# Performance work log

Hardware: AMD Instinct MI355X
Metric: run time of the kernel (lower is better)

## Reference

```python
import jax, jax.numpy as jnp
import numpy as np

B, C, F_IN, F_OUT = 4096, 63, 250, 250
NEG_SLOPE = 0.2  # GATConv default negative_slope


def setup_inputs() -> dict:
    key = jax.random.key(0)
    ks = jax.random.split(key, 5)
    return {
        "x": jax.random.normal(ks[0], (B, 1, C, F_IN), dtype=jnp.float32),
        "W": jax.random.normal(ks[1], (F_IN, F_OUT), dtype=jnp.float32) / np.sqrt(F_IN),
        "att_src": jax.random.normal(ks[2], (F_OUT,), dtype=jnp.float32) / np.sqrt(F_OUT),
        "att_dst": jax.random.normal(ks[3], (F_OUT,), dtype=jnp.float32) / np.sqrt(F_OUT),
        "bias": jax.random.normal(ks[4], (F_OUT,), dtype=jnp.float32) * 0.01,
    }


def reference(x, W, att_src, att_dst, bias):
    # x: [B, 1, C, F_in] -> per-batch graph of C=63 nodes, fully connected
    # (all i!=j edges plus GATConv's default self-loops => dense C x C attention).
    h = jnp.einsum("bcf,fo->bco", x[:, 0], W)          # [B, C, F_out] node embeddings
    a_s = jnp.einsum("bco,o->bc", h, att_src)           # per-source score
    a_d = jnp.einsum("bco,o->bc", h, att_dst)           # per-destination score
    # e[b, dst, src] = leakyrelu(a_s[src] + a_d[dst]); softmax over sources per dst
    e = jax.nn.leaky_relu(a_s[:, None, :] + a_d[:, :, None], NEG_SLOPE)  # [B, C, C]
    alpha = jax.nn.softmax(e, axis=-1)
    out = jnp.einsum("bds,bso->bdo", alpha, h) + bias   # [B, C, F_out]
    return out[:, None]                                  # [B, 1, C, F_out]
```

## Files before the change

### kernel.cpp

```cpp
#include <hip/hip_runtime.h>
#include <hip/hip_bf16.h>

typedef __bf16 bf16;
typedef __attribute__((ext_vector_type(8))) __bf16 bf16x8;
typedef __attribute__((ext_vector_type(4))) __bf16 bf16x4;
typedef __attribute__((ext_vector_type(2))) __bf16 bf16x2;
typedef __attribute__((ext_vector_type(4))) float f32x4;

#define C_NODES 63
#define F_DIM   250
#define NEG_SLOPE 0.2f

#define OFF_AS    32000
#define OFF_AD    32256
#define OFF_ALPHA 32768
#define LDS_BYTES 40960

__device__ __forceinline__ int swz(int a) { return a ^ ((a >> 3) & 0x70); }
__device__ __forceinline__ int swzA(int a) {
    return a ^ ((((a >> 8) & 3) ^ ((a >> 10) & 3)) << 4) ^ (((a >> 12) & 1) << 6);
}

extern "C" __global__ __launch_bounds__(256)
void gat_prep(const float* __restrict__ W, const float* __restrict__ att_src,
              const float* __restrict__ att_dst, bf16* __restrict__ Wp) {
    int i = blockIdx.x * 256 + threadIdx.x;
    int tile = i >> 9;
    int ln   = (i >> 3) & 63;
    int j    = i & 7;
    int kt = tile >> 4, nt = tile & 15;
    int k = kt * 32 + (ln >> 4) * 8 + j;
    int n = nt * 16 + (ln & 15);
    float v = 0.f;
    if (k < F_DIM) {
        if (n < F_DIM) {
            v = W[k * F_DIM + n];
        } else if (n == F_DIM || n == F_DIM + 1) {
            const float* att = (n == F_DIM) ? att_src : att_dst;
            float s = 0.f;
            for (int o = 0; o < F_DIM; ++o) s = fmaf(W[k * F_DIM + o], att[o], s);
            v = s;
        }
    }
    Wp[i] = (bf16)v;
}

extern "C" __global__ __launch_bounds__(512, 8)
void gat_main(const float* __restrict__ x, const bf16* __restrict__ Wp,
              const float* __restrict__ bias, float* __restrict__ out)
{
    __shared__ __align__(16) unsigned char smem[LDS_BYTES];
    const int tid  = threadIdx.x;
    const int lane = tid & 63;
    const int w    = tid >> 6;
    const int b    = blockIdx.x;
    const int fl   = lane & 15;
    const int fh   = lane >> 4;

    const bf16x8* wpv = (const bf16x8*)Wp;

    if (tid < 64) {
        int base = swzA((((tid >> 4) * 8 + 7) << 10) + (48 + (tid & 15)) * 16);
        *(unsigned int*)(smem + base + 4) = 0u;
        *(unsigned long long*)(smem + base + 8) = 0ull;
    } else if (tid < 96) {
        int idx = tid - 64;
        int base = swzA(((24 + (idx >> 2)) << 10) + ((((idx & 3) << 4) | 15) * 16));
        *(f32x4*)(smem + base) = (f32x4){0.f, 0.f, 0.f, 0.f};
    }

    {
        const float* xb = x + (size_t)b * (C_NODES * F_DIM);
#pragma unroll
        for (int it = 0; it < 4; ++it) {
            int idx = tid + it * 512;
            if (idx < 2016) {
                int r = idx >> 5, g = idx & 31;
                const float* src = xb + r * F_DIM + g * 8;
                int dl = (r & 15) | ((g & 3) << 4);
                int base = swzA((((r >> 4) * 8 + (g >> 2)) << 10) + dl * 16);
                if (g < 31) {
                    float2 v0 = *(const float2*)(src);
                    float2 v1 = *(const float2*)(src + 2);
                    float2 v2 = *(const float2*)(src + 4);
                    float2 v3 = *(const float2*)(src + 6);
                    bf16x8 pk = { (bf16)v0.x, (bf16)v0.y, (bf16)v1.x, (bf16)v1.y,
                                  (bf16)v2.x, (bf16)v2.y, (bf16)v3.x, (bf16)v3.y };
                    *(bf16x8*)(smem + base) = pk;
                } else {
                    float2 v0 = *(const float2*)(src);
                    bf16x2 pk = { (bf16)v0.x, (bf16)v0.y };
                    *(bf16x2*)(smem + base) = pk;
                }
            }
        }
    }
    __syncthreads();

    f32x4 acc[4][2];
#pragma unroll
    for (int mt = 0; mt < 4; ++mt) {
        acc[mt][0] = (f32x4){0.f, 0.f, 0.f, 0.f};
        acc[mt][1] = (f32x4){0.f, 0.f, 0.f, 0.f};
    }
#pragma unroll 1
    for (int kt = 0; kt < 8; ++kt) {
        bf16x8 bw0 = wpv[(kt * 16 + w * 2)     * 64 + lane];
        bf16x8 bw1 = wpv[(kt * 16 + w * 2 + 1) * 64 + lane];
#pragma unroll
        for (int mt = 0; mt < 4; ++mt) {
            bf16x8 af = *(const bf16x8*)(smem + swzA(((mt * 8 + kt) << 10) + lane * 16));
            acc[mt][0] = __builtin_amdgcn_mfma_f32_16x16x32_bf16(af, bw0, acc[mt][0], 0, 0, 0);
            acc[mt][1] = __builtin_amdgcn_mfma_f32_16x16x32_bf16(af, bw1, acc[mt][1], 0, 0, 0);
        }
    }
    __syncthreads();

    {
#pragma unroll
        for (int mt = 0; mt < 4; ++mt) {
            int s0 = mt * 16 + fh * 4;
#pragma unroll
            for (int nti = 0; nti < 2; ++nti) {
                int f = w * 32 + nti * 16 + fl;
                if (f < F_DIM) {
                    f32x4 v = acc[mt][nti];
                    bf16x4 hv = { (bf16)v.x, (bf16)v.y, (bf16)v.z, (bf16)v.w };
                    *(bf16x4*)(smem + swz(f * 128 + s0 * 2)) = hv;
                }
            }
        }
        if (w == 7 && (fl == 10 || fl == 11)) {
            float* dst = (float*)(smem + (fl == 10 ? OFF_AS : OFF_AD));
#pragma unroll
            for (int mt = 0; mt < 4; ++mt) {
                f32x4 v = acc[mt][1];
#pragma unroll
                for (int i = 0; i < 4; ++i) dst[mt * 16 + fh * 4 + i] = v[i];
            }
        }
    }
    __syncthreads();

    {
        const float* AS  = (const float*)(smem + OFF_AS);
        const float* ADp = (const float*)(smem + OFF_AD);
        int d = tid >> 3;
        int c = tid & 7;
        float ad_v = ADp[d];
        f32x4 a0 = *(const f32x4*)(AS + c * 8);
        f32x4 a1 = *(const f32x4*)(AS + c * 8 + 4);
        float p[8];
#pragma unroll
        for (int k = 0; k < 4; ++k) {
            float e;
            e = a0[k] + ad_v; p[k]     = (e > 0.f) ? e : NEG_SLOPE * e;
            e = a1[k] + ad_v; p[4 + k] = (e > 0.f) ? e : NEG_SLOPE * e;
        }
        if (c == 7) p[7] = -3.0e38f;
        float md = p[0];
#pragma unroll
        for (int k = 1; k < 8; ++k) md = fmaxf(md, p[k]);
        md = fmaxf(md, __shfl_xor(md, 1));
        md = fmaxf(md, __shfl_xor(md, 2));
        md = fmaxf(md, __shfl_xor(md, 4));
        float sum = 0.f;
#pragma unroll
        for (int k = 0; k < 8; ++k) { p[k] = __expf(p[k] - md); sum += p[k]; }
        sum += __shfl_xor(sum, 1);
        sum += __shfl_xor(sum, 2);
        sum += __shfl_xor(sum, 4);
        float rz = 1.f / sum;
        bf16x8 pk;
#pragma unroll
        for (int k = 0; k < 8; ++k) pk[k] = (bf16)(p[k] * rz);
        *(bf16x8*)(smem + swz(OFF_ALPHA + d * 128 + c * 16)) = pk;
    }
    __syncthreads();

    f32x4 acc2[4][2];
#pragma unroll
    for (int mt = 0; mt < 4; ++mt) {
        acc2[mt][0] = (f32x4){0.f, 0.f, 0.f, 0.f};
        acc2[mt][1] = (f32x4){0.f, 0.f, 0.f, 0.f};
    }
#pragma unroll 1
    for (int ks = 0; ks < 2; ++ks) {
        int kk = ks * 32 + fh * 8;
        bf16x8 hbf0, hbf1;
        {
            int f0 = w * 32 + fl;
            int f1 = f0 + 16;
            hbf0 = *(const bf16x8*)(smem + swz(f0 * 128 + kk * 2));
            hbf1 = *(const bf16x8*)(smem + swz(f1 * 128 + kk * 2));
        }
#pragma unroll
        for (int mt = 0; mt < 4; ++mt) {
            bf16x8 aal = *(const bf16x8*)(smem + swz(OFF_ALPHA + (mt * 16 + fl) * 128 + kk * 2));
            acc2[mt][0] = __builtin_amdgcn_mfma_f32_16x16x32_bf16(aal, hbf0, acc2[mt][0], 0, 0, 0);
            acc2[mt][1] = __builtin_amdgcn_mfma_f32_16x16x32_bf16(aal, hbf1, acc2[mt][1], 0, 0, 0);
        }
    }

    float bv[2];
#pragma unroll
    for (int nti = 0; nti < 2; ++nti) {
        int f = w * 32 + nti * 16 + fl;
        bv[nti] = (f < F_DIM) ? bias[f] : 0.f;
    }
    float* ob = out + (size_t)b * (C_NODES * F_DIM);
#pragma unroll
    for (int mt = 0; mt < 4; ++mt) {
#pragma unroll
        for (int i = 0; i < 4; ++i) {
            int r = mt * 16 + fh * 4 + i;
            if (r < C_NODES) {
#pragma unroll
                for (int nti = 0; nti < 2; ++nti) {
                    int f = w * 32 + nti * 16 + fl;
                    if (f < F_DIM) ob[r * F_DIM + f] = acc2[mt][nti][i] + bv[nti];
                }
            }
        }
    }
}

extern "C" void kernel_launch(void* const* d_in, const int* in_sizes, int n_in,
                              void* d_out, int out_size, void* d_ws, size_t ws_size,
                              hipStream_t stream) {
    const float* x       = (const float*)d_in[0];
    const float* W       = (const float*)d_in[1];
    const float* att_src = (const float*)d_in[2];
    const float* att_dst = (const float*)d_in[3];
    const float* bias    = (const float*)d_in[4];
    float* out = (float*)d_out;
    bf16* Wp = (bf16*)d_ws;

    gat_prep<<<256, 256, 0, stream>>>(W, att_src, att_dst, Wp);
    gat_main<<<4096, 512, 0, stream>>>(x, Wp, bias, out);
}
```

Measured before the change: 145.5 us.

## Keep h and attention in registers via cross-lane shuffles, dropping LDS round trips

```diff
diff --git a/kernel.cpp b/kernel.cpp
--- a/kernel.cpp
+++ b/kernel.cpp
@@ -3,20 +3,16 @@
 
 typedef __bf16 bf16;
 typedef __attribute__((ext_vector_type(8))) __bf16 bf16x8;
-typedef __attribute__((ext_vector_type(4))) __bf16 bf16x4;
 typedef __attribute__((ext_vector_type(2))) __bf16 bf16x2;
 typedef __attribute__((ext_vector_type(4))) float f32x4;
+typedef __attribute__((ext_vector_type(4))) unsigned int uint4v;
 
 #define C_NODES 63
 #define F_DIM   250
 #define NEG_SLOPE 0.2f
 
-#define OFF_AS    32000
-#define OFF_AD    32256
-#define OFF_ALPHA 32768
-#define LDS_BYTES 40960
-
-__device__ __forceinline__ int swz(int a) { return a ^ ((a >> 3) & 0x70); }
+#define LDS_BYTES 32768
+
 __device__ __forceinline__ int swzA(int a) {
     return a ^ ((((a >> 8) & 3) ^ ((a >> 10) & 3)) << 4) ^ (((a >> 12) & 1) << 6);
 }
@@ -45,7 +41,7 @@
     Wp[i] = (bf16)v;
 }
 
-extern "C" __global__ __launch_bounds__(512, 8)
+extern "C" __global__ __launch_bounds__(512, 4)
 void gat_main(const float* __restrict__ x, const bf16* __restrict__ Wp,
               const float* __restrict__ bias, float* __restrict__ out)
 {
@@ -84,13 +80,13 @@
                     float2 v1 = *(const float2*)(src + 2);
                     float2 v2 = *(const float2*)(src + 4);
                     float2 v3 = *(const float2*)(src + 6);
-                    bf16x8 pk = { (bf16)v0.x, (bf16)v0.y, (bf16)v1.x, (bf16)v1.y,
-                                  (bf16)v2.x, (bf16)v2.y, (bf16)v3.x, (bf16)v3.y };
-                    *(bf16x8*)(smem + base) = pk;
+                    bf16x8 pk8 = { (bf16)v0.x, (bf16)v0.y, (bf16)v1.x, (bf16)v1.y,
+                                   (bf16)v2.x, (bf16)v2.y, (bf16)v3.x, (bf16)v3.y };
+                    *(bf16x8*)(smem + base) = pk8;
                 } else {
                     float2 v0 = *(const float2*)(src);
-                    bf16x2 pk = { (bf16)v0.x, (bf16)v0.y };
-                    *(bf16x2*)(smem + base) = pk;
+                    bf16x2 pk2 = { (bf16)v0.x, (bf16)v0.y };
+                    *(bf16x2*)(smem + base) = pk2;
                 }
             }
         }
@@ -98,107 +94,120 @@
     __syncthreads();
 
     f32x4 acc[4][2];
+    f32x4 acc15[4];
 #pragma unroll
     for (int mt = 0; mt < 4; ++mt) {
         acc[mt][0] = (f32x4){0.f, 0.f, 0.f, 0.f};
         acc[mt][1] = (f32x4){0.f, 0.f, 0.f, 0.f};
+        acc15[mt]  = (f32x4){0.f, 0.f, 0.f, 0.f};
     }
 #pragma unroll 1
     for (int kt = 0; kt < 8; ++kt) {
         bf16x8 bw0 = wpv[(kt * 16 + w * 2)     * 64 + lane];
         bf16x8 bw1 = wpv[(kt * 16 + w * 2 + 1) * 64 + lane];
+        bf16x8 bwS = wpv[(kt * 16 + 15)        * 64 + lane];
 #pragma unroll
         for (int mt = 0; mt < 4; ++mt) {
             bf16x8 af = *(const bf16x8*)(smem + swzA(((mt * 8 + kt) << 10) + lane * 16));
             acc[mt][0] = __builtin_amdgcn_mfma_f32_16x16x32_bf16(af, bw0, acc[mt][0], 0, 0, 0);
             acc[mt][1] = __builtin_amdgcn_mfma_f32_16x16x32_bf16(af, bw1, acc[mt][1], 0, 0, 0);
-        }
-    }
-    __syncthreads();
-
+            acc15[mt]  = __builtin_amdgcn_mfma_f32_16x16x32_bf16(af, bwS, acc15[mt], 0, 0, 0);
+        }
+    }
+
+    unsigned int pk[4][2][2];
+#pragma unroll
+    for (int mt = 0; mt < 4; ++mt)
+#pragma unroll
+        for (int nti = 0; nti < 2; ++nti) {
+            f32x4 v = acc[mt][nti];
+            bf16x2 p0 = { (bf16)v.x, (bf16)v.y };
+            bf16x2 p1 = { (bf16)v.z, (bf16)v.w };
+            pk[mt][nti][0] = __builtin_bit_cast(unsigned int, p0);
+            pk[mt][nti][1] = __builtin_bit_cast(unsigned int, p1);
+        }
+
+    const int LA = ((fh & 1) << 5) + fl;
+    const int LB = LA + 16;
+    const bool fhHi = (fh & 2) != 0;
+    uint4v hb[2][2];
+#pragma unroll
+    for (int nti = 0; nti < 2; ++nti)
+#pragma unroll
+        for (int kt2 = 0; kt2 < 2; ++kt2) {
+            unsigned int u[4];
+#pragma unroll
+            for (int h = 0; h < 2; ++h) {
+                unsigned int a0 = __shfl(pk[kt2 * 2][nti][h],     LA);
+                unsigned int a1 = __shfl(pk[kt2 * 2 + 1][nti][h], LA);
+                u[h] = fhHi ? a1 : a0;
+                unsigned int b0 = __shfl(pk[kt2 * 2][nti][h],     LB);
+                unsigned int b1 = __shfl(pk[kt2 * 2 + 1][nti][h], LB);
+                u[2 + h] = fhHi ? b1 : b0;
+            }
+            hb[nti][kt2] = (uint4v){u[0], u[1], u[2], u[3]};
+        }
+
+    float asv[16];
+#pragma unroll
+    for (int kt2 = 0; kt2 < 2; ++kt2)
+#pragma unroll
+        for (int j = 0; j < 8; ++j) {
+            int Ls = (((fh & 1) * 2 + (j >> 2)) << 4) + 10;
+            float c0 = __shfl(acc15[kt2 * 2][j & 3],     Ls);
+            float c1 = __shfl(acc15[kt2 * 2 + 1][j & 3], Ls);
+            asv[kt2 * 8 + j] = fhHi ? c1 : c0;
+        }
+    float adv[4];
     {
+        int Ld = ((fl >> 2) << 4) + 11;
 #pragma unroll
         for (int mt = 0; mt < 4; ++mt) {
-            int s0 = mt * 16 + fh * 4;
-#pragma unroll
-            for (int nti = 0; nti < 2; ++nti) {
-                int f = w * 32 + nti * 16 + fl;
-                if (f < F_DIM) {
-                    f32x4 v = acc[mt][nti];
-                    bf16x4 hv = { (bf16)v.x, (bf16)v.y, (bf16)v.z, (bf16)v.w };
-                    *(bf16x4*)(smem + swz(f * 128 + s0 * 2)) = hv;
-                }
-            }
-        }
-        if (w == 7 && (fl == 10 || fl == 11)) {
-            float* dst = (float*)(smem + (fl == 10 ? OFF_AS : OFF_AD));
-#pragma unroll
-            for (int mt = 0; mt < 4; ++mt) {
-                f32x4 v = acc[mt][1];
-#pragma unroll
-                for (int i = 0; i < 4; ++i) dst[mt * 16 + fh * 4 + i] = v[i];
-            }
-        }
-    }
-    __syncthreads();
-
-    {
-        const float* AS  = (const float*)(smem + OFF_AS);
-        const float* ADp = (const float*)(smem + OFF_AD);
-        int d = tid >> 3;
-        int c = tid & 7;
-        float ad_v = ADp[d];
-        f32x4 a0 = *(const f32x4*)(AS + c * 8);
-        f32x4 a1 = *(const f32x4*)(AS + c * 8 + 4);
-        float p[8];
-#pragma unroll
-        for (int k = 0; k < 4; ++k) {
-            float e;
-            e = a0[k] + ad_v; p[k]     = (e > 0.f) ? e : NEG_SLOPE * e;
-            e = a1[k] + ad_v; p[4 + k] = (e > 0.f) ? e : NEG_SLOPE * e;
-        }
-        if (c == 7) p[7] = -3.0e38f;
+            float t0 = __shfl(acc15[mt][0], Ld);
+            float t1 = __shfl(acc15[mt][1], Ld);
+            float t2 = __shfl(acc15[mt][2], Ld);
+            float t3 = __shfl(acc15[mt][3], Ld);
+            float s01 = (fl & 1) ? t1 : t0;
+            float s23 = (fl & 1) ? t3 : t2;
+            adv[mt] = (fl & 2) ? s23 : s01;
+        }
+    }
+
+    f32x4 acc2[4][2];
+#pragma unroll
+    for (int mt = 0; mt < 4; ++mt) {
+        float p[16];
+#pragma unroll
+        for (int k = 0; k < 16; ++k) {
+            float e = asv[k] + adv[mt];
+            p[k] = (e > 0.f) ? e : NEG_SLOPE * e;
+        }
+        if (fh == 3) p[15] = -3.0e38f;
         float md = p[0];
 #pragma unroll
-        for (int k = 1; k < 8; ++k) md = fmaxf(md, p[k]);
-        md = fmaxf(md, __shfl_xor(md, 1));
-        md = fmaxf(md, __shfl_xor(md, 2));
-        md = fmaxf(md, __shfl_xor(md, 4));
+        for (int k = 1; k < 16; ++k) md = fmaxf(md, p[k]);
+        md = fmaxf(md, __shfl_xor(md, 16));
+        md = fmaxf(md, __shfl_xor(md, 32));
         float sum = 0.f;
 #pragma unroll
-        for (int k = 0; k < 8; ++k) { p[k] = __expf(p[k] - md); sum += p[k]; }
-        sum += __shfl_xor(sum, 1);
-        sum += __shfl_xor(sum, 2);
-        sum += __shfl_xor(sum, 4);
+        for (int k = 0; k < 16; ++k) { p[k] = __expf(p[k] - md); sum += p[k]; }
+        sum += __shfl_xor(sum, 16);
+        sum += __shfl_xor(sum, 32);
         float rz = 1.f / sum;
-        bf16x8 pk;
-#pragma unroll
-        for (int k = 0; k < 8; ++k) pk[k] = (bf16)(p[k] * rz);
-        *(bf16x8*)(smem + swz(OFF_ALPHA + d * 128 + c * 16)) = pk;
-    }
-    __syncthreads();
-
-    f32x4 acc2[4][2];
-#pragma unroll
-    for (int mt = 0; mt < 4; ++mt) {
+        bf16x8 aal0, aal1;
+#pragma unroll
+        for (int k = 0; k < 8; ++k) {
+            aal0[k] = (bf16)(p[k] * rz);
+            aal1[k] = (bf16)(p[8 + k] * rz);
+        }
         acc2[mt][0] = (f32x4){0.f, 0.f, 0.f, 0.f};
         acc2[mt][1] = (f32x4){0.f, 0.f, 0.f, 0.f};
-    }
-#pragma unroll 1
-    for (int ks = 0; ks < 2; ++ks) {
-        int kk = ks * 32 + fh * 8;
-        bf16x8 hbf0, hbf1;
-        {
-            int f0 = w * 32 + fl;
-            int f1 = f0 + 16;
-            hbf0 = *(const bf16x8*)(smem + swz(f0 * 128 + kk * 2));
-            hbf1 = *(const bf16x8*)(smem + swz(f1 * 128 + kk * 2));
-        }
-#pragma unroll
-        for (int mt = 0; mt < 4; ++mt) {
-            bf16x8 aal = *(const bf16x8*)(smem + swz(OFF_ALPHA + (mt * 16 + fl) * 128 + kk * 2));
-            acc2[mt][0] = __builtin_amdgcn_mfma_f32_16x16x32_bf16(aal, hbf0, acc2[mt][0], 0, 0, 0);
-            acc2[mt][1] = __builtin_amdgcn_mfma_f32_16x16x32_bf16(aal, hbf1, acc2[mt][1], 0, 0, 0);
+#pragma unroll
+        for (int nti = 0; nti < 2; ++nti) {
+            bf16x8 h0 = __builtin_bit_cast(bf16x8, hb[nti][0]);
+            bf16x8 h1 = __builtin_bit_cast(bf16x8, hb[nti][1]);
+            acc2[mt][nti] = __builtin_amdgcn_mfma_f32_16x16x32_bf16(aal0, h0, acc2[mt][nti], 0, 0, 0);
+            acc2[mt][nti] = __builtin_amdgcn_mfma_f32_16x16x32_bf16(aal1, h1, acc2[mt][nti], 0, 0, 0);
         }
     }
 
```

Result: slower. 164.5 us (+13.1%).

## Process eight batches per persistent block with register prefetch of next x

Applied to the files above, without the earlier changes.

```diff
diff --git a/kernel.cpp b/kernel.cpp
--- a/kernel.cpp
+++ b/kernel.cpp
@@ -10,15 +10,24 @@
 #define C_NODES 63
 #define F_DIM   250
 #define NEG_SLOPE 0.2f
-
-#define OFF_AS    32000
-#define OFF_AD    32256
-#define OFF_ALPHA 32768
-#define LDS_BYTES 40960
+#define BS 8
+
+#define AFR_B     0
+#define HSB       32768
+#define OFF_AS    64768
+#define OFF_AD    65024
+#define ALPHA_B   65280
+#define LDS_BYTES 73472
 
 __device__ __forceinline__ int swz(int a) { return a ^ ((a >> 3) & 0x70); }
 __device__ __forceinline__ int swzA(int a) {
     return a ^ ((((a >> 8) & 3) ^ ((a >> 10) & 3)) << 4) ^ (((a >> 12) & 1) << 6);
+}
+
+__device__ __forceinline__ void barrier_lds() {
+    asm volatile("s_waitcnt lgkmcnt(0)" ::: "memory");
+    __builtin_amdgcn_s_barrier();
+    __builtin_amdgcn_sched_barrier(0);
 }
 
 extern "C" __global__ __launch_bounds__(256)
@@ -45,7 +54,7 @@
     Wp[i] = (bf16)v;
 }
 
-extern "C" __global__ __launch_bounds__(512, 8)
+extern "C" __global__ __launch_bounds__(512, 4)
 void gat_main(const float* __restrict__ x, const bf16* __restrict__ Wp,
               const float* __restrict__ bias, float* __restrict__ out)
 {
@@ -53,9 +62,9 @@
     const int tid  = threadIdx.x;
     const int lane = tid & 63;
     const int w    = tid >> 6;
-    const int b    = blockIdx.x;
     const int fl   = lane & 15;
     const int fh   = lane >> 4;
+    const int b0   = blockIdx.x * BS;
 
     const bf16x8* wpv = (const bf16x8*)Wp;
 
@@ -69,8 +78,12 @@
         *(f32x4*)(smem + base) = (f32x4){0.f, 0.f, 0.f, 0.f};
     }
 
+    float bv0, bv1;
+    { int f = w * 32 + fl;      bv0 = (f < F_DIM) ? bias[f] : 0.f;
+      f += 16;                  bv1 = (f < F_DIM) ? bias[f] : 0.f; }
+
     {
-        const float* xb = x + (size_t)b * (C_NODES * F_DIM);
+        const float* xb = x + (size_t)b0 * (C_NODES * F_DIM);
 #pragma unroll
         for (int it = 0; it < 4; ++it) {
             int idx = tid + it * 512;
@@ -84,39 +97,61 @@
                     float2 v1 = *(const float2*)(src + 2);
                     float2 v2 = *(const float2*)(src + 4);
                     float2 v3 = *(const float2*)(src + 6);
-                    bf16x8 pk = { (bf16)v0.x, (bf16)v0.y, (bf16)v1.x, (bf16)v1.y,
-                                  (bf16)v2.x, (bf16)v2.y, (bf16)v3.x, (bf16)v3.y };
-                    *(bf16x8*)(smem + base) = pk;
+                    bf16x8 pk8 = { (bf16)v0.x, (bf16)v0.y, (bf16)v1.x, (bf16)v1.y,
+                                   (bf16)v2.x, (bf16)v2.y, (bf16)v3.x, (bf16)v3.y };
+                    *(bf16x8*)(smem + base) = pk8;
                 } else {
                     float2 v0 = *(const float2*)(src);
-                    bf16x2 pk = { (bf16)v0.x, (bf16)v0.y };
-                    *(bf16x2*)(smem + base) = pk;
-                }
-            }
-        }
-    }
-    __syncthreads();
-
-    f32x4 acc[4][2];
-#pragma unroll
-    for (int mt = 0; mt < 4; ++mt) {
-        acc[mt][0] = (f32x4){0.f, 0.f, 0.f, 0.f};
-        acc[mt][1] = (f32x4){0.f, 0.f, 0.f, 0.f};
-    }
+                    bf16x2 pk2 = { (bf16)v0.x, (bf16)v0.y };
+                    *(bf16x2*)(smem + base) = pk2;
+                }
+            }
+        }
+    }
+
+    float2 pf[4][4];
+    {
+        const float* xb = x + (size_t)(b0 + 1) * (C_NODES * F_DIM);
+#pragma unroll
+        for (int it = 0; it < 4; ++it) {
+            int idx = tid + it * 512;
+            if (idx < 2016) {
+                int r = idx >> 5, g = idx & 31;
+                const float* src = xb + r * F_DIM + g * 8;
+                pf[it][0] = *(const float2*)(src);
+                if (g < 31) {
+                    pf[it][1] = *(const float2*)(src + 2);
+                    pf[it][2] = *(const float2*)(src + 4);
+                    pf[it][3] = *(const float2*)(src + 6);
+                }
+            }
+        }
+    }
+    barrier_lds();
+
 #pragma unroll 1
-    for (int kt = 0; kt < 8; ++kt) {
-        bf16x8 bw0 = wpv[(kt * 16 + w * 2)     * 64 + lane];
-        bf16x8 bw1 = wpv[(kt * 16 + w * 2 + 1) * 64 + lane];
+    for (int i = 0; i < BS; ++i) {
+        const int b = b0 + i;
+
+        f32x4 acc[4][2];
 #pragma unroll
         for (int mt = 0; mt < 4; ++mt) {
-            bf16x8 af = *(const bf16x8*)(smem + swzA(((mt * 8 + kt) << 10) + lane * 16));
-            acc[mt][0] = __builtin_amdgcn_mfma_f32_16x16x32_bf16(af, bw0, acc[mt][0], 0, 0, 0);
-            acc[mt][1] = __builtin_amdgcn_mfma_f32_16x16x32_bf16(af, bw1, acc[mt][1], 0, 0, 0);
-        }
-    }
-    __syncthreads();
-
-    {
+            acc[mt][0] = (f32x4){0.f, 0.f, 0.f, 0.f};
+            acc[mt][1] = (f32x4){0.f, 0.f, 0.f, 0.f};
+        }
+#pragma unroll 1
+        for (int kt = 0; kt < 8; ++kt) {
+            bf16x8 bw0 = wpv[(kt * 16 + w * 2)     * 64 + lane];
+            bf16x8 bw1 = wpv[(kt * 16 + w * 2 + 1) * 64 + lane];
+#pragma unroll
+            for (int mt = 0; mt < 4; ++mt) {
+                bf16x8 af = *(const bf16x8*)(smem + swzA(((mt * 8 + kt) << 10) + lane * 16));
+                acc[mt][0] = __builtin_amdgcn_mfma_f32_16x16x32_bf16(af, bw0, acc[mt][0], 0, 0, 0);
+                acc[mt][1] = __builtin_amdgcn_mfma_f32_16x16x32_bf16(af, bw1, acc[mt][1], 0, 0, 0);
+            }
+        }
+        barrier_lds();
+
 #pragma unroll
         for (int mt = 0; mt < 4; ++mt) {
             int s0 = mt * 16 + fh * 4;
@@ -126,7 +161,7 @@
                 if (f < F_DIM) {
                     f32x4 v = acc[mt][nti];
                     bf16x4 hv = { (bf16)v.x, (bf16)v.y, (bf16)v.z, (bf16)v.w };
-                    *(bf16x4*)(smem + swz(f * 128 + s0 * 2)) = hv;
+                    *(bf16x4*)(smem + swz(HSB + f * 128 + s0 * 2)) = hv;
                 }
             }
         }
@@ -136,89 +171,114 @@
             for (int mt = 0; mt < 4; ++mt) {
                 f32x4 v = acc[mt][1];
 #pragma unroll
-                for (int i = 0; i < 4; ++i) dst[mt * 16 + fh * 4 + i] = v[i];
-            }
-        }
-    }
-    __syncthreads();
-
-    {
-        const float* AS  = (const float*)(smem + OFF_AS);
-        const float* ADp = (const float*)(smem + OFF_AD);
-        int d = tid >> 3;
-        int c = tid & 7;
-        float ad_v = ADp[d];
-        f32x4 a0 = *(const f32x4*)(AS + c * 8);
-        f32x4 a1 = *(const f32x4*)(AS + c * 8 + 4);
-        float p[8];
-#pragma unroll
-        for (int k = 0; k < 4; ++k) {
-            float e;
-            e = a0[k] + ad_v; p[k]     = (e > 0.f) ? e : NEG_SLOPE * e;
-            e = a1[k] + ad_v; p[4 + k] = (e > 0.f) ? e : NEG_SLOPE * e;
-        }
-        if (c == 7) p[7] = -3.0e38f;
-        float md = p[0];
-#pragma unroll
-        for (int k = 1; k < 8; ++k) md = fmaxf(md, p[k]);
-        md = fmaxf(md, __shfl_xor(md, 1));
-        md = fmaxf(md, __shfl_xor(md, 2));
-        md = fmaxf(md, __shfl_xor(md, 4));
-        float sum = 0.f;
-#pragma unroll
-        for (int k = 0; k < 8; ++k) { p[k] = __expf(p[k] - md); sum += p[k]; }
-        sum += __shfl_xor(sum, 1);
-        sum += __shfl_xor(sum, 2);
-        sum += __shfl_xor(sum, 4);
-        float rz = 1.f / sum;
-        bf16x8 pk;
-#pragma unroll
-        for (int k = 0; k < 8; ++k) pk[k] = (bf16)(p[k] * rz);
-        *(bf16x8*)(smem + swz(OFF_ALPHA + d * 128 + c * 16)) = pk;
-    }
-    __syncthreads();
-
-    f32x4 acc2[4][2];
-#pragma unroll
-    for (int mt = 0; mt < 4; ++mt) {
-        acc2[mt][0] = (f32x4){0.f, 0.f, 0.f, 0.f};
-        acc2[mt][1] = (f32x4){0.f, 0.f, 0.f, 0.f};
-    }
+                for (int q = 0; q < 4; ++q) dst[mt * 16 + fh * 4 + q] = v[q];
+            }
+        }
+        if (i + 1 < BS) {
+#pragma unroll
+            for (int it = 0; it < 4; ++it) {
+                int idx = tid + it * 512;
+                if (idx < 2016) {
+                    int r = idx >> 5, g = idx & 31;
+                    int dl = (r & 15) | ((g & 3) << 4);
+                    int base = swzA((((r >> 4) * 8 + (g >> 2)) << 10) + dl * 16);
+                    if (g < 31) {
+                        bf16x8 pk8 = { (bf16)pf[it][0].x, (bf16)pf[it][0].y,
+                                       (bf16)pf[it][1].x, (bf16)pf[it][1].y,
+                                       (bf16)pf[it][2].x, (bf16)pf[it][2].y,
+                                       (bf16)pf[it][3].x, (bf16)pf[it][3].y };
+                        *(bf16x8*)(smem + base) = pk8;
+                    } else {
+                        bf16x2 pk2 = { (bf16)pf[it][0].x, (bf16)pf[it][0].y };
+                        *(bf16x2*)(smem + base) = pk2;
+                    }
+                }
+            }
+            if (i + 2 < BS) {
+                const float* xb = x + (size_t)(b0 + i + 2) * (C_NODES * F_DIM);
+#pragma unroll
+                for (int it = 0; it < 4; ++it) {
+                    int idx = tid + it * 512;
+                    if (idx < 2016) {
+                        int r = idx >> 5, g = idx & 31;
+                        const float* src = xb + r * F_DIM + g * 8;
+                        pf[it][0] = *(const float2*)(src);
+                        if (g < 31) {
+                            pf[it][1] = *(const float2*)(src + 2);
+                            pf[it][2] = *(const float2*)(src + 4);
+                            pf[it][3] = *(const float2*)(src + 6);
+                        }
+                    }
+                }
+            }
+        }
+        barrier_lds();
+
+        {
+            const float* AS  = (const float*)(smem + OFF_AS);
+            const float* ADp = (const float*)(smem + OFF_AD);
+            int d = tid >> 3;
+            int c = tid & 7;
+            float ad_v = ADp[d];
+            f32x4 a0 = *(const f32x4*)(AS + c * 8);
+            f32x4 a1 = *(const f32x4*)(AS + c * 8 + 4);
+            float p[8];
+#pragma unroll
+            for (int k = 0; k < 4; ++k) {
+                float e;
+                e = a0[k] + ad_v; p[k]     = (e > 0.f) ? e : NEG_SLOPE * e;
+                e = a1[k] + ad_v; p[4 + k] = (e > 0.f) ? e : NEG_SLOPE * e;
+            }
+            if (c == 7) p[7] = -3.0e38f;
+            float md = p[0];
+#pragma unroll
+            for (int k = 1; k < 8; ++k) md = fmaxf(md, p[k]);
+            md = fmaxf(md, __shfl_xor(md, 1));
+            md = fmaxf(md, __shfl_xor(md, 2));
+            md = fmaxf(md, __shfl_xor(md, 4));
+            float sum = 0.f;
+#pragma unroll
+            for (int k = 0; k < 8; ++k) { p[k] = __expf(p[k] - md); sum += p[k]; }
+            sum += __shfl_xor(sum, 1);
+            sum += __shfl_xor(sum, 2);
+            sum += __shfl_xor(sum, 4);
+            float rz = 1.f / sum;
+            bf16x8 pk;
+#pragma unroll
+            for (int k = 0; k < 8; ++k) pk[k] = (bf16)(p[k] * rz);
+            *(bf16x8*)(smem + swz(ALPHA_B + d * 128 + c * 16)) = pk;
+        }
+        barrier_lds();
+
+        f32x4 acc2[4][2];
+#pragma unroll
+        for (int mt = 0; mt < 4; ++mt) {
+            acc2[mt][0] = (f32x4){0.f, 0.f, 0.f, 0.f};
+            acc2[mt][1] = (f32x4){0.f, 0.f, 0.f, 0.f};
+        }
 #pragma unroll 1
-    for (int ks = 0; ks < 2; ++ks) {
-        int kk = ks * 32 + fh * 8;
-        bf16x8 hbf0, hbf1;
-        {
-            int f0 = w * 32 + fl;
-            int f1 = f0 + 16;
-            hbf0 = *(const bf16x8*)(smem + swz(f0 * 128 + kk * 2));
-            hbf1 = *(const bf16x8*)(smem + swz(f1 * 128 + kk * 2));
-        }
+        for (int ks = 0; ks < 2; ++ks) {
+            int kk = ks * 32 + fh * 8;
+            bf16x8 hbf0 = *(const bf16x8*)(smem + swz(HSB + (w * 32 + fl)      * 128 + kk * 2));
+            bf16x8 hbf1 = *(const bf16x8*)(smem + swz(HSB + (w * 32 + fl + 16) * 128 + kk * 2));
+#pragma unroll
+            for (int mt = 0; mt < 4; ++mt) {
+                bf16x8 aal = *(const bf16x8*)(smem + swz(ALPHA_B + (mt * 16 + fl) * 128 + kk * 2));
+                acc2[mt][0] = __builtin_amdgcn_mfma_f32_16x16x32_bf16(aal, hbf0, acc2[mt][0], 0, 0, 0);
+                acc2[mt][1] = __builtin_amdgcn_mfma_f32_16x16x32_bf16(aal, hbf1, acc2[mt][1], 0, 0, 0);
+            }
+        }
+        float* ob = out + (size_t)b * (C_NODES * F_DIM);
 #pragma unroll
         for (int mt = 0; mt < 4; ++mt) {
-            bf16x8 aal = *(const bf16x8*)(smem + swz(OFF_ALPHA + (mt * 16 + fl) * 128 + kk * 2));
-            acc2[mt][0] = __builtin_amdgcn_mfma_f32_16x16x32_bf16(aal, hbf0, acc2[mt][0], 0, 0, 0);
-            acc2[mt][1] = __builtin_amdgcn_mfma_f32_16x16x32_bf16(aal, hbf1, acc2[mt][1], 0, 0, 0);
-        }
-    }
-
-    float bv[2];
-#pragma unroll
-    for (int nti = 0; nti < 2; ++nti) {
-        int f = w * 32 + nti * 16 + fl;
-        bv[nti] = (f < F_DIM) ? bias[f] : 0.f;
-    }
-    float* ob = out + (size_t)b * (C_NODES * F_DIM);
-#pragma unroll
-    for (int mt = 0; mt < 4; ++mt) {
-#pragma unroll
-        for (int i = 0; i < 4; ++i) {
-            int r = mt * 16 + fh * 4 + i;
-            if (r < C_NODES) {
-#pragma unroll
-                for (int nti = 0; nti < 2; ++nti) {
-                    int f = w * 32 + nti * 16 + fl;
-                    if (f < F_DIM) ob[r * F_DIM + f] = acc2[mt][nti][i] + bv[nti];
+#pragma unroll
+            for (int q = 0; q < 4; ++q) {
+                int r = mt * 16 + fh * 4 + q;
+                if (r < C_NODES) {
+                    int f = w * 32 + fl;
+                    ob[r * F_DIM + f] = acc2[mt][0][q] + bv0;
+                    f += 16;
+                    if (f < F_DIM) ob[r * F_DIM + f] = acc2[mt][1][q] + bv1;
                 }
             }
         }
@@ -237,5 +297,5 @@
     bf16* Wp = (bf16*)d_ws;
 
     gat_prep<<<256, 256, 0, stream>>>(W, att_src, att_dst, Wp);
-    gat_main<<<4096, 512, 0, stream>>>(x, Wp, bias, out);
-}
+    gat_main<<<512, 512, 0, stream>>>(x, Wp, bias, out);
+}
```

After: 207.6 us. +42.6%, slower.

## Process 8 batches per block with async global-to-LDS prefetch of next x

Applied to the files above, without the earlier changes.

```diff
diff --git a/kernel.cpp b/kernel.cpp
--- a/kernel.cpp
+++ b/kernel.cpp
@@ -3,22 +3,34 @@
 
 typedef __bf16 bf16;
 typedef __attribute__((ext_vector_type(8))) __bf16 bf16x8;
-typedef __attribute__((ext_vector_type(4))) __bf16 bf16x4;
 typedef __attribute__((ext_vector_type(2))) __bf16 bf16x2;
 typedef __attribute__((ext_vector_type(4))) float f32x4;
+typedef __attribute__((ext_vector_type(4))) unsigned int uint4v;
 
 #define C_NODES 63
 #define F_DIM   250
 #define NEG_SLOPE 0.2f
-
-#define OFF_AS    32000
-#define OFF_AD    32256
-#define OFF_ALPHA 32768
-#define LDS_BYTES 40960
+#define BS 8
+
+#define ROWB      1040
+#define SLAB      0
+#define OFF_AS    65536
+#define OFF_AD    65792
+#define ALPHA_B   66048
+#define LDS_BYTES 74240
 
 __device__ __forceinline__ int swz(int a) { return a ^ ((a >> 3) & 0x70); }
-__device__ __forceinline__ int swzA(int a) {
-    return a ^ ((((a >> 8) & 3) ^ ((a >> 10) & 3)) << 4) ^ (((a >> 12) & 1) << 6);
+
+typedef const __attribute__((address_space(1))) void* gas_t;
+typedef __attribute__((address_space(3))) void* las_t;
+__device__ __forceinline__ void dma16(const void* g, void* l) {
+    __builtin_amdgcn_global_load_lds((gas_t)g, (las_t)l, 16, 0, 0);
+}
+
+__device__ __forceinline__ void bar_lgkm() {
+    asm volatile("s_waitcnt lgkmcnt(0)" ::: "memory");
+    __builtin_amdgcn_s_barrier();
+    __builtin_amdgcn_sched_barrier(0);
 }
 
 extern "C" __global__ __launch_bounds__(256)
@@ -45,7 +57,7 @@
     Wp[i] = (bf16)v;
 }
 
-extern "C" __global__ __launch_bounds__(512, 8)
+extern "C" __global__ __launch_bounds__(512, 4)
 void gat_main(const float* __restrict__ x, const bf16* __restrict__ Wp,
               const float* __restrict__ bias, float* __restrict__ out)
 {
@@ -53,81 +65,79 @@
     const int tid  = threadIdx.x;
     const int lane = tid & 63;
     const int w    = tid >> 6;
-    const int b    = blockIdx.x;
     const int fl   = lane & 15;
     const int fh   = lane >> 4;
+    const int b0   = blockIdx.x * BS;
 
     const bf16x8* wpv = (const bf16x8*)Wp;
 
-    if (tid < 64) {
-        int base = swzA((((tid >> 4) * 8 + 7) << 10) + (48 + (tid & 15)) * 16);
-        *(unsigned int*)(smem + base + 4) = 0u;
-        *(unsigned long long*)(smem + base + 8) = 0ull;
-    } else if (tid < 96) {
-        int idx = tid - 64;
-        int base = swzA(((24 + (idx >> 2)) << 10) + ((((idx & 3) << 4) | 15) * 16));
-        *(f32x4*)(smem + base) = (f32x4){0.f, 0.f, 0.f, 0.f};
+    float bv0, bv1;
+    { int f = w * 32 + fl;      bv0 = (f < F_DIM) ? bias[f] : 0.f;
+      f += 16;                  bv1 = (f < F_DIM) ? bias[f] : 0.f; }
+
+    if (tid < 63) {
+        *(unsigned long long*)(smem + SLAB + tid * ROWB + 1000) = 0ull;
+        *(f32x4*)(smem + SLAB + tid * ROWB + 1008) = (f32x4){0.f, 0.f, 0.f, 0.f};
     }
 
     {
-        const float* xb = x + (size_t)b * (C_NODES * F_DIM);
-#pragma unroll
-        for (int it = 0; it < 4; ++it) {
-            int idx = tid + it * 512;
-            if (idx < 2016) {
-                int r = idx >> 5, g = idx & 31;
-                const float* src = xb + r * F_DIM + g * 8;
-                int dl = (r & 15) | ((g & 3) << 4);
-                int base = swzA((((r >> 4) * 8 + (g >> 2)) << 10) + dl * 16);
-                if (g < 31) {
-                    float2 v0 = *(const float2*)(src);
-                    float2 v1 = *(const float2*)(src + 2);
-                    float2 v2 = *(const float2*)(src + 4);
-                    float2 v3 = *(const float2*)(src + 6);
-                    bf16x8 pk = { (bf16)v0.x, (bf16)v0.y, (bf16)v1.x, (bf16)v1.y,
-                                  (bf16)v2.x, (bf16)v2.y, (bf16)v3.x, (bf16)v3.y };
-                    *(bf16x8*)(smem + base) = pk;
+        const float* xb = x + (size_t)b0 * (C_NODES * F_DIM);
+        float2 tl = {0.f, 0.f};
+        if (tid < 63) tl = *(const float2*)(xb + tid * F_DIM + 248);
+#pragma unroll
+        for (int rr = 0; rr < 8; ++rr) {
+            int r = w * 8 + rr;
+            if (r < 63 && lane < 62)
+                dma16(xb + r * F_DIM + lane * 4, smem + SLAB + r * ROWB);
+        }
+        if (tid < 63) *(float2*)(smem + SLAB + tid * ROWB + 992) = tl;
+    }
+    asm volatile("s_waitcnt vmcnt(0)" ::: "memory");
+    bar_lgkm();
+
+#pragma unroll 1
+    for (int i = 0; i < BS; ++i) {
+        const int b = b0 + i;
+        const float* xnext = x + (size_t)(b + 1) * (C_NODES * F_DIM);
+
+        float2 tl = {0.f, 0.f};
+        if (i + 1 < BS && tid < 63) tl = *(const float2*)(xnext + tid * F_DIM + 248);
+
+        f32x4 acc[4][2];
+#pragma unroll
+        for (int mt = 0; mt < 4; ++mt) {
+            acc[mt][0] = (f32x4){0.f, 0.f, 0.f, 0.f};
+            acc[mt][1] = (f32x4){0.f, 0.f, 0.f, 0.f};
+        }
+#pragma unroll 1
+        for (int kt = 0; kt < 8; ++kt) {
+            bf16x8 bw0 = wpv[(kt * 16 + w * 2)     * 64 + lane];
+            bf16x8 bw1 = wpv[(kt * 16 + w * 2 + 1) * 64 + lane];
+#pragma unroll
+            for (int mt = 0; mt < 4; ++mt) {
+                int row = mt * 16 + fl;
+                bf16x8 af;
+                if (row < C_NODES) {
+                    const f32x4* p = (const f32x4*)(smem + SLAB + row * ROWB + kt * 128 + fh * 32);
+                    f32x4 lo = p[0], hi = p[1];
+                    af = (bf16x8){ (bf16)lo.x, (bf16)lo.y, (bf16)lo.z, (bf16)lo.w,
+                                   (bf16)hi.x, (bf16)hi.y, (bf16)hi.z, (bf16)hi.w };
                 } else {
-                    float2 v0 = *(const float2*)(src);
-                    bf16x2 pk = { (bf16)v0.x, (bf16)v0.y };
-                    *(bf16x2*)(smem + base) = pk;
+                    af = (bf16x8){(bf16)0.f,(bf16)0.f,(bf16)0.f,(bf16)0.f,
+                                  (bf16)0.f,(bf16)0.f,(bf16)0.f,(bf16)0.f};
                 }
-            }
-        }
-    }
-    __syncthreads();
-
-    f32x4 acc[4][2];
-#pragma unroll
-    for (int mt = 0; mt < 4; ++mt) {
-        acc[mt][0] = (f32x4){0.f, 0.f, 0.f, 0.f};
-        acc[mt][1] = (f32x4){0.f, 0.f, 0.f, 0.f};
-    }
-#pragma unroll 1
-    for (int kt = 0; kt < 8; ++kt) {
-        bf16x8 bw0 = wpv[(kt * 16 + w * 2)     * 64 + lane];
-        bf16x8 bw1 = wpv[(kt * 16 + w * 2 + 1) * 64 + lane];
-#pragma unroll
-        for (int mt = 0; mt < 4; ++mt) {
-            bf16x8 af = *(const bf16x8*)(smem + swzA(((mt * 8 + kt) << 10) + lane * 16));
-            acc[mt][0] = __builtin_amdgcn_mfma_f32_16x16x32_bf16(af, bw0, acc[mt][0], 0, 0, 0);
-            acc[mt][1] = __builtin_amdgcn_mfma_f32_16x16x32_bf16(af, bw1, acc[mt][1], 0, 0, 0);
-        }
-    }
-    __syncthreads();
-
-    {
-#pragma unroll
-        for (int mt = 0; mt < 4; ++mt) {
-            int s0 = mt * 16 + fh * 4;
-#pragma unroll
-            for (int nti = 0; nti < 2; ++nti) {
-                int f = w * 32 + nti * 16 + fl;
-                if (f < F_DIM) {
-                    f32x4 v = acc[mt][nti];
-                    bf16x4 hv = { (bf16)v.x, (bf16)v.y, (bf16)v.z, (bf16)v.w };
-                    *(bf16x4*)(smem + swz(f * 128 + s0 * 2)) = hv;
-                }
+                acc[mt][0] = __builtin_amdgcn_mfma_f32_16x16x32_bf16(af, bw0, acc[mt][0], 0, 0, 0);
+                acc[mt][1] = __builtin_amdgcn_mfma_f32_16x16x32_bf16(af, bw1, acc[mt][1], 0, 0, 0);
+            }
+        }
+        bar_lgkm();
+
+        if (i + 1 < BS) {
+#pragma unroll
+            for (int rr = 0; rr < 8; ++rr) {
+                int r = w * 8 + rr;
+                if (r < 63 && lane < 62)
+                    dma16(xnext + r * F_DIM + lane * 4, smem + SLAB + r * ROWB);
             }
         }
         if (w == 7 && (fl == 10 || fl == 11)) {
@@ -136,91 +146,115 @@
             for (int mt = 0; mt < 4; ++mt) {
                 f32x4 v = acc[mt][1];
 #pragma unroll
-                for (int i = 0; i < 4; ++i) dst[mt * 16 + fh * 4 + i] = v[i];
-            }
-        }
-    }
-    __syncthreads();
-
-    {
-        const float* AS  = (const float*)(smem + OFF_AS);
-        const float* ADp = (const float*)(smem + OFF_AD);
-        int d = tid >> 3;
-        int c = tid & 7;
-        float ad_v = ADp[d];
-        f32x4 a0 = *(const f32x4*)(AS + c * 8);
-        f32x4 a1 = *(const f32x4*)(AS + c * 8 + 4);
-        float p[8];
-#pragma unroll
-        for (int k = 0; k < 4; ++k) {
-            float e;
-            e = a0[k] + ad_v; p[k]     = (e > 0.f) ? e : NEG_SLOPE * e;
-            e = a1[k] + ad_v; p[4 + k] = (e > 0.f) ? e : NEG_SLOPE * e;
-        }
-        if (c == 7) p[7] = -3.0e38f;
-        float md = p[0];
-#pragma unroll
-        for (int k = 1; k < 8; ++k) md = fmaxf(md, p[k]);
-        md = fmaxf(md, __shfl_xor(md, 1));
-        md = fmaxf(md, __shfl_xor(md, 2));
-        md = fmaxf(md, __shfl_xor(md, 4));
-        float sum = 0.f;
-#pragma unroll
-        for (int k = 0; k < 8; ++k) { p[k] = __expf(p[k] - md); sum += p[k]; }
-        sum += __shfl_xor(sum, 1);
-        sum += __shfl_xor(sum, 2);
-        sum += __shfl_xor(sum, 4);
-        float rz = 1.f / sum;
-        bf16x8 pk;
-#pragma unroll
-        for (int k = 0; k < 8; ++k) pk[k] = (bf16)(p[k] * rz);
-        *(bf16x8*)(smem + swz(OFF_ALPHA + d * 128 + c * 16)) = pk;
-    }
-    __syncthreads();
-
-    f32x4 acc2[4][2];
-#pragma unroll
-    for (int mt = 0; mt < 4; ++mt) {
-        acc2[mt][0] = (f32x4){0.f, 0.f, 0.f, 0.f};
-        acc2[mt][1] = (f32x4){0.f, 0.f, 0.f, 0.f};
-    }
-#pragma unroll 1
-    for (int ks = 0; ks < 2; ++ks) {
-        int kk = ks * 32 + fh * 8;
-        bf16x8 hbf0, hbf1;
+                for (int q = 0; q < 4; ++q) dst[mt * 16 + fh * 4 + q] = v[q];
+            }
+        }
+        unsigned int pk[4][2][2];
+#pragma unroll
+        for (int mt = 0; mt < 4; ++mt)
+#pragma unroll
+            for (int nti = 0; nti < 2; ++nti) {
+                f32x4 v = acc[mt][nti];
+                bf16x2 p0 = { (bf16)v.x, (bf16)v.y };
+                bf16x2 p1 = { (bf16)v.z, (bf16)v.w };
+                pk[mt][nti][0] = __builtin_bit_cast(unsigned int, p0);
+                pk[mt][nti][1] = __builtin_bit_cast(unsigned int, p1);
+            }
+        const int LA = ((fh & 1) << 5) + fl;
+        const int LB = LA + 16;
+        const bool fhHi = (fh & 2) != 0;
+        uint4v hb[2][2];
+#pragma unroll
+        for (int nti = 0; nti < 2; ++nti)
+#pragma unroll
+            for (int kt2 = 0; kt2 < 2; ++kt2) {
+                unsigned int u[4];
+#pragma unroll
+                for (int h = 0; h < 2; ++h) {
+                    unsigned int a0 = __shfl(pk[kt2 * 2][nti][h],     LA);
+                    unsigned int a1 = __shfl(pk[kt2 * 2 + 1][nti][h], LA);
+                    u[h] = fhHi ? a1 : a0;
+                    unsigned int c0 = __shfl(pk[kt2 * 2][nti][h],     LB);
+                    unsigned int c1 = __shfl(pk[kt2 * 2 + 1][nti][h], LB);
+                    u[2 + h] = fhHi ? c1 : c0;
+                }
+                hb[nti][kt2] = (uint4v){u[0], u[1], u[2], u[3]};
+            }
+        if (i + 1 < BS && tid < 63)
+            *(float2*)(smem + SLAB + tid * ROWB + 992) = tl;
+        bar_lgkm();
+
         {
-            int f0 = w * 32 + fl;
-            int f1 = f0 + 16;
-            hbf0 = *(const bf16x8*)(smem + swz(f0 * 128 + kk * 2));
-            hbf1 = *(const bf16x8*)(smem + swz(f1 * 128 + kk * 2));
-        }
+            const float* AS  = (const float*)(smem + OFF_AS);
+            const float* ADp = (const float*)(smem + OFF_AD);
+            int d = tid >> 3;
+            int c = tid & 7;
+            float ad_v = ADp[d];
+            f32x4 a0 = *(const f32x4*)(AS + c * 8);
+            f32x4 a1 = *(const f32x4*)(AS + c * 8 + 4);
+            float p[8];
+#pragma unroll
+            for (int k = 0; k < 4; ++k) {
+                float e;
+                e = a0[k] + ad_v; p[k]     = (e > 0.f) ? e : NEG_SLOPE * e;
+                e = a1[k] + ad_v; p[4 + k] = (e > 0.f) ? e : NEG_SLOPE * e;
+            }
+            if (c == 7) p[7] = -3.0e38f;
+            float md = p[0];
+#pragma unroll
+            for (int k = 1; k < 8; ++k) md = fmaxf(md, p[k]);
+            md = fmaxf(md, __shfl_xor(md, 1));
+            md = fmaxf(md, __shfl_xor(md, 2));
+            md = fmaxf(md, __shfl_xor(md, 4));
+            float sum = 0.f;
+#pragma unroll
+            for (int k = 0; k < 8; ++k) { p[k] = __expf(p[k] - md); sum += p[k]; }
+            sum += __shfl_xor(sum, 1);
+            sum += __shfl_xor(sum, 2);
+            sum += __shfl_xor(sum, 4);
+            float rz = 1.f / sum;
+            bf16x8 pkv;
+#pragma unroll
+            for (int k = 0; k < 8; ++k) pkv[k] = (bf16)(p[k] * rz);
+            *(bf16x8*)(smem + swz(ALPHA_B + d * 128 + c * 16)) = pkv;
+        }
+        bar_lgkm();
+
+        f32x4 acc2[4][2];
 #pragma unroll
         for (int mt = 0; mt < 4; ++mt) {
-            bf16x8 aal = *(const bf16x8*)(smem + swz(OFF_ALPHA + (mt * 16 + fl) * 128 + kk * 2));
-            acc2[mt][0] = __builtin_amdgcn_mfma_f32_16x16x32_bf16(aal, hbf0, acc2[mt][0], 0, 0, 0);
-            acc2[mt][1] = __builtin_amdgcn_mfma_f32_16x16x32_bf16(aal, hbf1, acc2[mt][1], 0, 0, 0);
-        }
-    }
-
-    float bv[2];
-#pragma unroll
-    for (int nti = 0; nti < 2; ++nti) {
-        int f = w * 32 + nti * 16 + fl;
-        bv[nti] = (f < F_DIM) ? bias[f] : 0.f;
-    }
-    float* ob = out + (size_t)b * (C_NODES * F_DIM);
-#pragma unroll
-    for (int mt = 0; mt < 4; ++mt) {
-#pragma unroll
-        for (int i = 0; i < 4; ++i) {
-            int r = mt * 16 + fh * 4 + i;
-            if (r < C_NODES) {
-#pragma unroll
-                for (int nti = 0; nti < 2; ++nti) {
-                    int f = w * 32 + nti * 16 + fl;
-                    if (f < F_DIM) ob[r * F_DIM + f] = acc2[mt][nti][i] + bv[nti];
+            acc2[mt][0] = (f32x4){0.f, 0.f, 0.f, 0.f};
+            acc2[mt][1] = (f32x4){0.f, 0.f, 0.f, 0.f};
+        }
+#pragma unroll
+        for (int ks = 0; ks < 2; ++ks) {
+            int kk = ks * 32 + fh * 8;
+            bf16x8 h0 = __builtin_bit_cast(bf16x8, hb[0][ks]);
+            bf16x8 h1 = __builtin_bit_cast(bf16x8, hb[1][ks]);
+#pragma unroll
+            for (int mt = 0; mt < 4; ++mt) {
+                bf16x8 aal = *(const bf16x8*)(smem + swz(ALPHA_B + (mt * 16 + fl) * 128 + kk * 2));
+                acc2[mt][0] = __builtin_amdgcn_mfma_f32_16x16x32_bf16(aal, h0, acc2[mt][0], 0, 0, 0);
+                acc2[mt][1] = __builtin_amdgcn_mfma_f32_16x16x32_bf16(aal, h1, acc2[mt][1], 0, 0, 0);
+            }
+        }
+        float* ob = out + (size_t)b * (C_NODES * F_DIM);
+#pragma unroll
+        for (int mt = 0; mt < 4; ++mt) {
+#pragma unroll
+            for (int q = 0; q < 4; ++q) {
+                int r = mt * 16 + fh * 4 + q;
+                if (r < C_NODES) {
+                    int f = w * 32 + fl;
+                    ob[r * F_DIM + f] = acc2[mt][0][q] + bv0;
+                    f += 16;
+                    if (f < F_DIM) ob[r * F_DIM + f] = acc2[mt][1][q] + bv1;
                 }
             }
+        }
+        if (i + 1 < BS) {
+            asm volatile("s_waitcnt vmcnt(32)" ::: "memory");
+            bar_lgkm();
         }
     }
 }
@@ -237,5 +271,5 @@
     bf16* Wp = (bf16*)d_ws;
 
     gat_prep<<<256, 256, 0, stream>>>(W, att_src, att_dst, Wp);
-    gat_main<<<4096, 512, 0, stream>>>(x, Wp, bias, out);
-}
+    gat_main<<<512, 512, 0, stream>>>(x, Wp, bias, out);
+}
```

New measurement: 137.9 us. -5.2%, faster.
